# Kernel tuning notes

Hardware: AMD Instinct MI355X
Metric: run time of the kernel (lower is better)

Reference implementation:

```python
import jax, jax.numpy as jnp
import numpy as np

G1 = 3.0  # cfg.TRAIN.IoU_Gamma1
G2 = 1.0  # cfg.TRAIN.IoU_Gamma2


def setup_inputs() -> dict:
    key = jax.random.key(0)
    ks = jax.random.split(key, 5)
    B, N = 16, 2048
    cls = 0.3 * jax.random.normal(ks[0], (B, N, 2), jnp.float32)
    label_cls = jax.random.randint(ks[1], (B, N), 0, 2).astype(jnp.int32)
    label_loc = jax.random.normal(ks[2], (B, 4, N), jnp.float32)
    pred_bboxes = jax.random.uniform(ks[3], (B, 4, N), jnp.float32)
    label_target = jax.random.uniform(ks[4], (B, 4), jnp.float32)
    dataset_id = jnp.zeros((B,), jnp.int32)
    return dict(cls=cls, label_cls=label_cls, label_loc=label_loc,
                pred_bboxes=pred_bboxes, label_target=label_target,
                dataset_id=dataset_id)


def _iou(boxes, target):
    # boxes [B,4,N] (x1,y1,x2,y2); target [B,4]
    x1, y1, x2, y2 = boxes[:, 0], boxes[:, 1], boxes[:, 2], boxes[:, 3]
    tx1, ty1, tx2, ty2 = (target[:, 0:1], target[:, 1:2],
                          target[:, 2:3], target[:, 3:4])
    ww = jnp.clip(jnp.minimum(tx2, x2) - jnp.maximum(tx1, x1), 0.0)
    hh = jnp.clip(jnp.minimum(ty2, y2) - jnp.maximum(ty1, y1), 0.0)
    area = (x2 - x1) * (y2 - y1)
    ta = (tx2 - tx1) * (ty2 - ty1)
    inter = ww * hh
    return inter / (area + ta - inter)  # [B,N]


def _forward(cls, label_loc, pred_bboxes, label_target, label_cls, dataset_id):
    prob = jnp.exp(cls[..., 1])                      # [B,N]
    pos = label_cls > 0                              # [B,N]
    iou = _iou(pred_bboxes, label_target)            # [B,N]
    # centerness distance to target center
    cx = label_loc[:, 0] + label_target[:, 0:1]      # [B,N]
    cy = label_loc[:, 1] + label_target[:, 1:2]
    tcx = (label_target[:, 0] + label_target[:, 2]) * 0.5
    tcy = (label_target[:, 1] + label_target[:, 3]) * 0.5
    d = jnp.sqrt((cx - tcx[:, None]) ** 2 + (cy - tcy[:, None]) ** 2)  # [B,N]
    # pair (p,q): both positive, d[q]-d[p] >= 1.0 (== nested sorted-loop selection)
    pair = (pos[:, :, None] & pos[:, None, :]
            & ((d[:, None, :] - d[:, :, None]) >= 1.0))               # [B,N,N]
    m = pair.astype(prob.dtype)
    cnt = m.sum((1, 2))                                               # [B]
    # guard exponent with the mask to avoid inf*0 on dead pairs
    e1 = jnp.where(pair, -G1 * (prob[:, :, None] - prob[:, None, :]), 0.0)
    iou_sg = jax.lax.stop_gradient(iou)
    e2 = jnp.where(pair, -G2 * (iou[:, :, None] - iou_sg[:, None, :]), 0.0)
    denom = jnp.maximum(cnt, 1.0)
    l1 = (jnp.exp(e1) * m).sum((1, 2)) / denom                        # [B]
    l2 = (jnp.exp(e2) * m).sum((1, 2)) / denom
    valid = ((dataset_id != 1) & (cnt > 0)).astype(prob.dtype)        # [B]
    nv = valid.sum()
    safe_nv = jnp.maximum(nv, 1.0)
    f1 = jnp.where(nv > 0, (l1 * valid).sum() / safe_nv, 0.0)
    f2 = jnp.where(nv > 0, (l2 * valid).sum() / safe_nv, 0.0)
    return (f1, f2)


def reference(cls, label_cls, label_loc, pred_bboxes, label_target, dataset_id):
    return _forward(cls, label_loc, pred_bboxes, label_target, label_cls, dataset_id)
```

## Files before the change

### kernel.cpp

```cpp
#include <hip/hip_runtime.h>


#define G1 3.0f
#define G2 1.0f

constexpr int B = 16;
constexpr int N = 2048;
constexpr int TI  = 1024;
constexpr int TJ  = 64;
constexpr int IPT = 4;
constexpr int ICH = N / TI;
constexpr int JCH = N / TJ;
constexpr int PB  = ICH * JCH;
constexpr int NBLK = B * PB;

__global__ void __launch_bounds__(256)
fused_pair_kernel(const float* __restrict__ cls,
                  const int*   __restrict__ label_cls,
                  const float* __restrict__ label_loc,
                  const float* __restrict__ pred,
                  const float* __restrict__ tgt,
                  double* __restrict__ part) {
  __shared__ float4 sj[TJ];
  __shared__ double red[3][4];

  const int bid = blockIdx.x;
  const int b   = bid >> 6;
  const int r   = bid & 63;
  const int ic  = r >> 5;
  const int jc  = r & 31;
  const int t   = threadIdx.x;
  const int base = b * N;

  const float tx1 = tgt[b * 4 + 0], ty1 = tgt[b * 4 + 1];
  const float tx2 = tgt[b * 4 + 2], ty2 = tgt[b * 4 + 3];
  const float ta  = (tx2 - tx1) * (ty2 - ty1);
  const float tcx = (tx1 + tx2) * 0.5f, tcy = (ty1 + ty2) * 0.5f;

  const float* __restrict__ pb = pred      + (size_t)b * 4 * N;
  const float* __restrict__ lb = label_loc + (size_t)b * 4 * N;

  auto elem = [&](int n, float& d, float& prob, float& iou, bool& pos) {
    float x1 = pb[n], y1 = pb[N + n], x2 = pb[2 * N + n], y2 = pb[3 * N + n];
    float ww = fmaxf(fminf(tx2, x2) - fmaxf(tx1, x1), 0.f);
    float hh = fmaxf(fminf(ty2, y2) - fmaxf(ty1, y1), 0.f);
    float inter = ww * hh;
    iou  = inter / ((x2 - x1) * (y2 - y1) + ta - inter);
    prob = __expf(cls[((size_t)(base + n)) * 2 + 1]);
    pos  = label_cls[base + n] > 0;
    float cx = lb[n] + tx1, cy = lb[N + n] + ty1;
    float dx = cx - tcx, dy = cy - tcy;
    d = sqrtf(dx * dx + dy * dy);
  };

  if (t < TJ) {
    float d, prob, iou; bool pos;
    elem(jc * TJ + t, d, prob, iou, pos);
    sj[t] = make_float4(pos ? d : -1e30f,
                        __expf(G1 * prob),
                        __expf(G2 * iou), 0.f);
  }

  float di[IPT], v1i[IPT], v2i[IPT], posi[IPT];
#pragma unroll
  for (int k = 0; k < IPT; ++k) {
    float d, prob, iou; bool pos;
    elem(ic * TI + k * 256 + t, d, prob, iou, pos);
    di[k]   = d;
    posi[k] = pos ? 1.f : 0.f;
    v1i[k]  = pos ? __expf(-G1 * prob) : 0.f;
    v2i[k]  = pos ? __expf(-G2 * iou)  : 0.f;
  }
  __syncthreads();

  float s1[IPT] = {}, s2[IPT] = {}, sc[IPT] = {};
#pragma unroll 8
  for (int q = 0; q < TJ; ++q) {
    const float4 j4 = sj[q];
#pragma unroll
    for (int k = 0; k < IPT; ++k) {
      float f = (j4.x - di[k] >= 1.0f) ? 1.0f : 0.0f;
      s1[k] = fmaf(f, j4.y, s1[k]);
      s2[k] = fmaf(f, j4.z, s2[k]);
      sc[k] += f;
    }
  }

  double p1 = 0, p2 = 0, pc = 0;
#pragma unroll
  for (int k = 0; k < IPT; ++k) {
    p1 += (double)v1i[k]  * (double)s1[k];
    p2 += (double)v2i[k]  * (double)s2[k];
    pc += (double)posi[k] * (double)sc[k];
  }

  for (int off = 32; off; off >>= 1) {
    p1 += __shfl_down(p1, off);
    p2 += __shfl_down(p2, off);
    pc += __shfl_down(pc, off);
  }
  const int wave = t >> 6, lane = t & 63;
  if (lane == 0) { red[0][wave] = p1; red[1][wave] = p2; red[2][wave] = pc; }
  __syncthreads();
  if (t == 0) {
    double a = 0, bb = 0, c = 0;
    for (int wv = 0; wv < 4; ++wv) { a += red[0][wv]; bb += red[1][wv]; c += red[2][wv]; }
    part[(size_t)bid * 3 + 0] = a;
    part[(size_t)bid * 3 + 1] = bb;
    part[(size_t)bid * 3 + 2] = c;
  }
}

__global__ void finalize_kernel(const double* __restrict__ part,
                                const int* __restrict__ dataset_id,
                                float* __restrict__ out) {
  __shared__ double sl1[B], sl2[B], sv[B];
  int t = threadIdx.x;
  int b = t >> 4, k = t & 15;

  double s1 = 0, s2 = 0, sc = 0;
  for (int q = 0; q < PB; q += 16) {
    size_t idx = (size_t)(b * PB + k + q) * 3;
    s1 += part[idx]; s2 += part[idx + 1]; sc += part[idx + 2];
  }
  for (int off = 8; off; off >>= 1) {
    s1 += __shfl_down(s1, off, 16);
    s2 += __shfl_down(s2, off, 16);
    sc += __shfl_down(sc, off, 16);
  }
  if (k == 0) {
    double denom = fmax(sc, 1.0);
    bool valid = (dataset_id[b] != 1) && (sc > 0.0);
    sl1[b] = valid ? s1 / denom : 0.0;
    sl2[b] = valid ? s2 / denom : 0.0;
    sv[b]  = valid ? 1.0 : 0.0;
  }
  __syncthreads();
  if (t == 0) {
    double nv = 0, f1 = 0, f2 = 0;
    for (int bb = 0; bb < B; ++bb) { nv += sv[bb]; f1 += sl1[bb]; f2 += sl2[bb]; }
    if (nv > 0) { f1 /= nv; f2 /= nv; } else { f1 = 0; f2 = 0; }
    out[0] = (float)f1;
    out[1] = (float)f2;
  }
}

extern "C" void kernel_launch(void* const* d_in, const int* in_sizes, int n_in,
                              void* d_out, int out_size, void* d_ws, size_t ws_size,
                              hipStream_t stream) {
  const float* cls       = (const float*)d_in[0];
  const int*   label_cls = (const int*)d_in[1];
  const float* label_loc = (const float*)d_in[2];
  const float* pred      = (const float*)d_in[3];
  const float* tgt       = (const float*)d_in[4];
  const int*   dset      = (const int*)d_in[5];

  double* part = (double*)d_ws;

  fused_pair_kernel<<<NBLK, 256, 0, stream>>>(cls, label_cls, label_loc,
                                              pred, tgt, part);
  finalize_kernel<<<1, 256, 0, stream>>>(part, dset, (float*)d_out);
}
```

Before: 19.52 us.

## Replace O(N^2) pair scan with per-tile sort, suffix sums and binary search

The all-pairs scan is replaced by a prep kernel that computes per-element values and, for each 128-element tile, sorts the masked distances by rank and writes suffix sums of the exp weights. A search kernel then binary-searches each tile for the d threshold, so each element does about log(128) work per tile instead of a full scan. The separate finalize launch is folded into the search kernel through an atomic last-block counter. This cuts the arithmetic from quadratic to roughly N*(N/128)*log. In exchange it adds an intermediate global round trip and a second launch that depends on the first, and it changes the float summation order.

```diff
diff --git a/kernel.cpp b/kernel.cpp
--- a/kernel.cpp
+++ b/kernel.cpp
@@ -4,33 +4,30 @@
 #define G1 3.0f
 #define G2 1.0f
 
-constexpr int B = 16;
-constexpr int N = 2048;
-constexpr int TI  = 1024;
-constexpr int TJ  = 64;
-constexpr int IPT = 4;
-constexpr int ICH = N / TI;
-constexpr int JCH = N / TJ;
-constexpr int PB  = ICH * JCH;
-constexpr int NBLK = B * PB;
-
-__global__ void __launch_bounds__(256)
-fused_pair_kernel(const float* __restrict__ cls,
-                  const int*   __restrict__ label_cls,
-                  const float* __restrict__ label_loc,
-                  const float* __restrict__ pred,
-                  const float* __restrict__ tgt,
-                  double* __restrict__ part) {
-  __shared__ float4 sj[TJ];
-  __shared__ double red[3][4];
-
-  const int bid = blockIdx.x;
-  const int b   = bid >> 6;
-  const int r   = bid & 63;
-  const int ic  = r >> 5;
-  const int jc  = r & 31;
-  const int t   = threadIdx.x;
-  const int base = b * N;
+constexpr int B  = 16;
+constexpr int N  = 2048;
+constexpr int TS = 128;
+constexpr int NT = N / TS;
+constexpr int K2S = 8;
+constexpr int K2B = B * K2S;
+
+
+__global__ void __launch_bounds__(TS)
+prep_kernel(const float* __restrict__ cls, const int* __restrict__ label_cls,
+            const float* __restrict__ label_loc, const float* __restrict__ pred,
+            const float* __restrict__ tgt,
+            float* __restrict__ dd, float* __restrict__ v1a, float* __restrict__ v2a,
+            float* __restrict__ ssd, float* __restrict__ suf1, float* __restrict__ suf2,
+            unsigned* __restrict__ counter) {
+  __shared__ uint4 stile[TS];
+
+  if (blockIdx.x == 0 && threadIdx.x == 0) *counter = 0u;
+
+  const int b  = blockIdx.x >> 4;
+  const int jc = blockIdx.x & (NT - 1);
+  const int t  = threadIdx.x;
+  const int n  = jc * TS + t;
+  const int gn = b * N + n;
 
   const float tx1 = tgt[b * 4 + 0], ty1 = tgt[b * 4 + 1];
   const float tx2 = tgt[b * 4 + 2], ty2 = tgt[b * 4 + 3];
@@ -40,108 +37,148 @@
   const float* __restrict__ pb = pred      + (size_t)b * 4 * N;
   const float* __restrict__ lb = label_loc + (size_t)b * 4 * N;
 
-  auto elem = [&](int n, float& d, float& prob, float& iou, bool& pos) {
-    float x1 = pb[n], y1 = pb[N + n], x2 = pb[2 * N + n], y2 = pb[3 * N + n];
-    float ww = fmaxf(fminf(tx2, x2) - fmaxf(tx1, x1), 0.f);
-    float hh = fmaxf(fminf(ty2, y2) - fmaxf(ty1, y1), 0.f);
-    float inter = ww * hh;
-    iou  = inter / ((x2 - x1) * (y2 - y1) + ta - inter);
-    prob = __expf(cls[((size_t)(base + n)) * 2 + 1]);
-    pos  = label_cls[base + n] > 0;
-    float cx = lb[n] + tx1, cy = lb[N + n] + ty1;
-    float dx = cx - tcx, dy = cy - tcy;
-    d = sqrtf(dx * dx + dy * dy);
-  };
-
-  if (t < TJ) {
-    float d, prob, iou; bool pos;
-    elem(jc * TJ + t, d, prob, iou, pos);
-    sj[t] = make_float4(pos ? d : -1e30f,
-                        __expf(G1 * prob),
-                        __expf(G2 * iou), 0.f);
-  }
-
-  float di[IPT], v1i[IPT], v2i[IPT], posi[IPT];
+  float x1 = pb[n], y1 = pb[N + n], x2 = pb[2 * N + n], y2 = pb[3 * N + n];
+  float ww = fmaxf(fminf(tx2, x2) - fmaxf(tx1, x1), 0.f);
+  float hh = fmaxf(fminf(ty2, y2) - fmaxf(ty1, y1), 0.f);
+  float inter = ww * hh;
+  float iou  = inter / ((x2 - x1) * (y2 - y1) + ta - inter);
+  float prob = __expf(cls[(size_t)gn * 2 + 1]);
+  bool  pos  = label_cls[gn] > 0;
+  float cx = lb[n] + tx1, cy = lb[N + n] + ty1;
+  float dx = cx - tcx, dy = cy - tcy;
+  float d  = sqrtf(dx * dx + dy * dy);
+
+  float dm = pos ? d : -1e30f;
+  float w1 = __expf(G1 * prob);
+  float w2 = __expf(G2 * iou);
+
+  dd[gn]  = d;
+  v1a[gn] = pos ? __expf(-G1 * prob) : 0.f;
+  v2a[gn] = pos ? __expf(-G2 * iou)  : 0.f;
+
+  unsigned u = __float_as_uint(dm);
+  u ^= (u & 0x80000000u) ? 0xFFFFFFFFu : 0x80000000u;
+  stile[t] = make_uint4((unsigned)t, u, __float_as_uint(w1), __float_as_uint(w2));
+  __syncthreads();
+
+  const unsigned long long mykey = ((unsigned long long)u << 32) | (unsigned)t;
+  int rank = 0;
+  float s1 = 0.f, s2 = 0.f;
+#pragma unroll 8
+  for (int q = 0; q < TS; ++q) {
+    uint4 v = stile[q];
+    unsigned long long kq = ((unsigned long long)v.y << 32) | v.x;
+    bool lt = kq < mykey;
+    rank += lt ? 1 : 0;
+    s1 += lt ? 0.f : __uint_as_float(v.z);
+    s2 += lt ? 0.f : __uint_as_float(v.w);
+  }
+  const int outp = b * N + jc * TS + rank;
+  ssd[outp]  = dm;
+  suf1[outp] = s1;
+  suf2[outp] = s2;
+}
+
+__global__ void __launch_bounds__(256)
+search_kernel(const float* __restrict__ dd, const float* __restrict__ v1a,
+              const float* __restrict__ v2a,
+              const float* __restrict__ ssd, const float* __restrict__ suf1,
+              const float* __restrict__ suf2,
+              const int* __restrict__ dataset_id,
+              double* __restrict__ part, unsigned* __restrict__ counter,
+              float* __restrict__ out) {
+  __shared__ float lsd[N], ls1[N], ls2[N];
+  __shared__ double red[3][4];
+  __shared__ double bl1[B], bl2[B], bval[B];
+  __shared__ unsigned s_last;
+
+  const int b  = blockIdx.x >> 3;
+  const int ib = blockIdx.x & (K2S - 1);
+  const int t  = threadIdx.x;
+
+  {
+    const float4* g1 = (const float4*)(ssd  + (size_t)b * N);
+    const float4* g2 = (const float4*)(suf1 + (size_t)b * N);
+    const float4* g3 = (const float4*)(suf2 + (size_t)b * N);
+    float4* p1l = (float4*)lsd; float4* p2l = (float4*)ls1; float4* p3l = (float4*)ls2;
 #pragma unroll
-  for (int k = 0; k < IPT; ++k) {
-    float d, prob, iou; bool pos;
-    elem(ic * TI + k * 256 + t, d, prob, iou, pos);
-    di[k]   = d;
-    posi[k] = pos ? 1.f : 0.f;
-    v1i[k]  = pos ? __expf(-G1 * prob) : 0.f;
-    v2i[k]  = pos ? __expf(-G2 * iou)  : 0.f;
-  }
-  __syncthreads();
-
-  float s1[IPT] = {}, s2[IPT] = {}, sc[IPT] = {};
-#pragma unroll 8
-  for (int q = 0; q < TJ; ++q) {
-    const float4 j4 = sj[q];
+    for (int r = 0; r < (N / 4) / 256; ++r) {
+      int idx = r * 256 + t;
+      p1l[idx] = g1[idx]; p2l[idx] = g2[idx]; p3l[idx] = g3[idx];
+    }
+  }
+
+  const int   i   = b * N + ib * 256 + t;
+  const float di  = dd[i];
+  const float v1i = v1a[i];
+  const float v2i = v2a[i];
+  __syncthreads();
+
+  double s1d = 0.0, s2d = 0.0;
+  int cnt = 0;
 #pragma unroll
-    for (int k = 0; k < IPT; ++k) {
-      float f = (j4.x - di[k] >= 1.0f) ? 1.0f : 0.0f;
-      s1[k] = fmaf(f, j4.y, s1[k]);
-      s2[k] = fmaf(f, j4.z, s2[k]);
-      sc[k] += f;
-    }
-  }
-
-  double p1 = 0, p2 = 0, pc = 0;
+  for (int tile = 0; tile < NT; ++tile) {
+    const int base = tile * TS;
+    int k = 0;
 #pragma unroll
-  for (int k = 0; k < IPT; ++k) {
-    p1 += (double)v1i[k]  * (double)s1[k];
-    p2 += (double)v2i[k]  * (double)s2[k];
-    pc += (double)posi[k] * (double)sc[k];
-  }
+    for (int w = TS >> 1; w > 0; w >>= 1)
+      k += (lsd[base + k + w - 1] - di >= 1.0f) ? 0 : w;
+    k += (lsd[base + k] - di >= 1.0f) ? 0 : 1;
+    const bool any = (k < TS);
+    const int  idx = base + (any ? k : 0);
+    s1d += (double)(any ? ls1[idx] : 0.f);
+    s2d += (double)(any ? ls2[idx] : 0.f);
+    cnt += TS - k;
+  }
+
+  double p1 = (double)v1i * s1d;
+  double p2 = (double)v2i * s2d;
+  double pc = (v1i > 0.f) ? (double)cnt : 0.0;
 
   for (int off = 32; off; off >>= 1) {
     p1 += __shfl_down(p1, off);
     p2 += __shfl_down(p2, off);
     pc += __shfl_down(pc, off);
   }
-  const int wave = t >> 6, lane = t & 63;
-  if (lane == 0) { red[0][wave] = p1; red[1][wave] = p2; red[2][wave] = pc; }
+  const int wv = t >> 6, lane = t & 63;
+  if (lane == 0) { red[0][wv] = p1; red[1][wv] = p2; red[2][wv] = pc; }
   __syncthreads();
   if (t == 0) {
-    double a = 0, bb = 0, c = 0;
-    for (int wv = 0; wv < 4; ++wv) { a += red[0][wv]; bb += red[1][wv]; c += red[2][wv]; }
-    part[(size_t)bid * 3 + 0] = a;
-    part[(size_t)bid * 3 + 1] = bb;
-    part[(size_t)bid * 3 + 2] = c;
-  }
-}
-
-__global__ void finalize_kernel(const double* __restrict__ part,
-                                const int* __restrict__ dataset_id,
-                                float* __restrict__ out) {
-  __shared__ double sl1[B], sl2[B], sv[B];
-  int t = threadIdx.x;
-  int b = t >> 4, k = t & 15;
-
-  double s1 = 0, s2 = 0, sc = 0;
-  for (int q = 0; q < PB; q += 16) {
-    size_t idx = (size_t)(b * PB + k + q) * 3;
-    s1 += part[idx]; s2 += part[idx + 1]; sc += part[idx + 2];
-  }
-  for (int off = 8; off; off >>= 1) {
-    s1 += __shfl_down(s1, off, 16);
-    s2 += __shfl_down(s2, off, 16);
-    sc += __shfl_down(sc, off, 16);
-  }
-  if (k == 0) {
-    double denom = fmax(sc, 1.0);
-    bool valid = (dataset_id[b] != 1) && (sc > 0.0);
-    sl1[b] = valid ? s1 / denom : 0.0;
-    sl2[b] = valid ? s2 / denom : 0.0;
-    sv[b]  = valid ? 1.0 : 0.0;
-  }
-  __syncthreads();
-  if (t == 0) {
-    double nv = 0, f1 = 0, f2 = 0;
-    for (int bb = 0; bb < B; ++bb) { nv += sv[bb]; f1 += sl1[bb]; f2 += sl2[bb]; }
-    if (nv > 0) { f1 /= nv; f2 /= nv; } else { f1 = 0; f2 = 0; }
-    out[0] = (float)f1;
-    out[1] = (float)f2;
+    part[(size_t)blockIdx.x * 3 + 0] = red[0][0] + red[0][1] + red[0][2] + red[0][3];
+    part[(size_t)blockIdx.x * 3 + 1] = red[1][0] + red[1][1] + red[1][2] + red[1][3];
+    part[(size_t)blockIdx.x * 3 + 2] = red[2][0] + red[2][1] + red[2][2] + red[2][3];
+    __threadfence();
+    unsigned old = atomicAdd(counter, 1u);
+    s_last = (old == (unsigned)(K2B - 1)) ? 1u : 0u;
+  }
+  __syncthreads();
+  if (s_last) {
+    __threadfence();
+    double q1 = 0, q2 = 0, qc = 0;
+    if (t < K2B) {
+      const volatile double* vp = part;
+      q1 = vp[t * 3 + 0]; q2 = vp[t * 3 + 1]; qc = vp[t * 3 + 2];
+    }
+    for (int off = 4; off; off >>= 1) {
+      q1 += __shfl_down(q1, off);
+      q2 += __shfl_down(q2, off);
+      qc += __shfl_down(qc, off);
+    }
+    if (t < K2B && (t & 7) == 0) {
+      int bb = t >> 3;
+      bool valid = (dataset_id[bb] != 1) && (qc > 0.0);
+      double denom = fmax(qc, 1.0);
+      bl1[bb]  = valid ? q1 / denom : 0.0;
+      bl2[bb]  = valid ? q2 / denom : 0.0;
+      bval[bb] = valid ? 1.0 : 0.0;
+    }
+    __syncthreads();
+    if (t == 0) {
+      double nv = 0, f1 = 0, f2 = 0;
+      for (int bb = 0; bb < B; ++bb) { nv += bval[bb]; f1 += bl1[bb]; f2 += bl2[bb]; }
+      out[0] = (float)((nv > 0) ? f1 / nv : 0.0);
+      out[1] = (float)((nv > 0) ? f2 / nv : 0.0);
+    }
   }
 }
 
@@ -155,9 +192,18 @@
   const float* tgt       = (const float*)d_in[4];
   const int*   dset      = (const int*)d_in[5];
 
-  double* part = (double*)d_ws;
-
-  fused_pair_kernel<<<NBLK, 256, 0, stream>>>(cls, label_cls, label_loc,
-                                              pred, tgt, part);
-  finalize_kernel<<<1, 256, 0, stream>>>(part, dset, (float*)d_out);
+  char*     ws      = (char*)d_ws;
+  unsigned* counter = (unsigned*)ws;
+  double*   part    = (double*)(ws + 64);
+  float*    dd      = (float*)(ws + 4096);
+  float*    v1a     = dd  + (size_t)B * N;
+  float*    v2a     = v1a + (size_t)B * N;
+  float*    ssd     = v2a + (size_t)B * N;
+  float*    suf1    = ssd + (size_t)B * N;
+  float*    suf2    = suf1 + (size_t)B * N;
+
+  prep_kernel<<<B * NT, TS, 0, stream>>>(cls, label_cls, label_loc, pred, tgt,
+                                         dd, v1a, v2a, ssd, suf1, suf2, counter);
+  search_kernel<<<K2B, 256, 0, stream>>>(dd, v1a, v2a, ssd, suf1, suf2,
+                                         dset, part, counter, (float*)d_out);
 }
```

Measured after the change: 27.57 us. 41.2% more time.

## Sort j-tile by distance with suffix sums and fuse finalize via last-block atomic

Applied to the files above, without the earlier changes.

Each 64-element j tile is now ranked by distance in shared memory, and suffix sums of the exp weights are built over that order. Each i element then binary-searches the threshold and reads one suffix sum, replacing the 64-iteration masked accumulation per i element. The separate finalize kernel is removed: the last block to arrive, found with an atomic counter, does the final reduction. The cost is a memset launch, a threadfence/atomic per block, and a sequential rank pass done by only 64 threads.

```diff
diff --git a/kernel.cpp b/kernel.cpp
--- a/kernel.cpp
+++ b/kernel.cpp
@@ -4,25 +4,27 @@
 #define G1 3.0f
 #define G2 1.0f
 
-constexpr int B = 16;
-constexpr int N = 2048;
-constexpr int TI  = 1024;
-constexpr int TJ  = 64;
-constexpr int IPT = 4;
-constexpr int ICH = N / TI;
-constexpr int JCH = N / TJ;
-constexpr int PB  = ICH * JCH;
-constexpr int NBLK = B * PB;
+constexpr int B    = 16;
+constexpr int N    = 2048;
+constexpr int TJ   = 64;
+constexpr int IPT  = 4;
+constexpr int TI   = 1024;
+constexpr int ICH  = N / TI;
+constexpr int JCH  = N / TJ;
+constexpr int NBLK = B * ICH * JCH;
 
 __global__ void __launch_bounds__(256)
-fused_pair_kernel(const float* __restrict__ cls,
-                  const int*   __restrict__ label_cls,
-                  const float* __restrict__ label_loc,
-                  const float* __restrict__ pred,
-                  const float* __restrict__ tgt,
-                  double* __restrict__ part) {
-  __shared__ float4 sj[TJ];
+igr_fused_kernel(const float* __restrict__ cls, const int* __restrict__ label_cls,
+                 const float* __restrict__ label_loc, const float* __restrict__ pred,
+                 const float* __restrict__ tgt, const int* __restrict__ dataset_id,
+                 double* __restrict__ part, unsigned* __restrict__ counter,
+                 float* __restrict__ out) {
+  __shared__ uint4  stile[TJ];
+  __shared__ float  ssd[TJ];
+  __shared__ float  suf1[TJ + 1], suf2[TJ + 1];
   __shared__ double red[3][4];
+  __shared__ double bl1[B], bl2[B], bval[B];
+  __shared__ unsigned s_last;
 
   const int bid = blockIdx.x;
   const int b   = bid >> 6;
@@ -53,95 +55,108 @@
     d = sqrtf(dx * dx + dy * dy);
   };
 
+  float dm_j = 0.f; unsigned uj = 0u;
   if (t < TJ) {
     float d, prob, iou; bool pos;
     elem(jc * TJ + t, d, prob, iou, pos);
-    sj[t] = make_float4(pos ? d : -1e30f,
-                        __expf(G1 * prob),
-                        __expf(G2 * iou), 0.f);
+    dm_j = pos ? d : -1e30f;
+    uj = __float_as_uint(dm_j);
+    uj ^= (uj & 0x80000000u) ? 0xFFFFFFFFu : 0x80000000u;
+    stile[t] = make_uint4(uj, (unsigned)t,
+                          __float_as_uint(__expf(G1 * prob)),
+                          __float_as_uint(__expf(G2 * iou)));
   }
+  if (t == TJ) { suf1[TJ] = 0.f; suf2[TJ] = 0.f; }
 
-  float di[IPT], v1i[IPT], v2i[IPT], posi[IPT];
+  float di[IPT], v1i[IPT], v2i[IPT];
 #pragma unroll
   for (int k = 0; k < IPT; ++k) {
     float d, prob, iou; bool pos;
     elem(ic * TI + k * 256 + t, d, prob, iou, pos);
-    di[k]   = d;
-    posi[k] = pos ? 1.f : 0.f;
-    v1i[k]  = pos ? __expf(-G1 * prob) : 0.f;
-    v2i[k]  = pos ? __expf(-G2 * iou)  : 0.f;
+    di[k]  = d;
+    v1i[k] = pos ? __expf(-G1 * prob) : 0.f;
+    v2i[k] = pos ? __expf(-G2 * iou)  : 0.f;
   }
   __syncthreads();
 
-  float s1[IPT] = {}, s2[IPT] = {}, sc[IPT] = {};
+  if (t < TJ) {
+    const unsigned long long mykey = ((unsigned long long)uj << 32) | (unsigned)t;
+    int rank = 0; float s1 = 0.f, s2 = 0.f;
 #pragma unroll 8
-  for (int q = 0; q < TJ; ++q) {
-    const float4 j4 = sj[q];
-#pragma unroll
-    for (int k = 0; k < IPT; ++k) {
-      float f = (j4.x - di[k] >= 1.0f) ? 1.0f : 0.0f;
-      s1[k] = fmaf(f, j4.y, s1[k]);
-      s2[k] = fmaf(f, j4.z, s2[k]);
-      sc[k] += f;
+    for (int q = 0; q < TJ; ++q) {
+      uint4 v = stile[q];
+      unsigned long long kq = ((unsigned long long)v.x << 32) | v.y;
+      bool lt = kq < mykey;
+      rank += lt ? 1 : 0;
+      s1 += lt ? 0.f : __uint_as_float(v.z);
+      s2 += lt ? 0.f : __uint_as_float(v.w);
     }
+    ssd[rank] = dm_j; suf1[rank] = s1; suf2[rank] = s2;
   }
+  __syncthreads();
 
-  double p1 = 0, p2 = 0, pc = 0;
+  double p1 = 0.0, p2 = 0.0; int cnt = 0;
 #pragma unroll
   for (int k = 0; k < IPT; ++k) {
-    p1 += (double)v1i[k]  * (double)s1[k];
-    p2 += (double)v2i[k]  * (double)s2[k];
-    pc += (double)posi[k] * (double)sc[k];
+    const float d = di[k];
+    int kk = 0;
+#pragma unroll
+    for (int w = TJ >> 1; w > 0; w >>= 1)
+      kk += (ssd[kk + w - 1] - d >= 1.0f) ? 0 : w;
+    kk += (ssd[kk] - d >= 1.0f) ? 0 : 1;
+    p1 += (double)v1i[k] * (double)suf1[kk];
+    p2 += (double)v2i[k] * (double)suf2[kk];
+    cnt += (v1i[k] > 0.f) ? (TJ - kk) : 0;
   }
+  double pc = (double)cnt;
 
   for (int off = 32; off; off >>= 1) {
     p1 += __shfl_down(p1, off);
     p2 += __shfl_down(p2, off);
     pc += __shfl_down(pc, off);
   }
-  const int wave = t >> 6, lane = t & 63;
-  if (lane == 0) { red[0][wave] = p1; red[1][wave] = p2; red[2][wave] = pc; }
+  const int wv = t >> 6, lane = t & 63;
+  if (lane == 0) { red[0][wv] = p1; red[1][wv] = p2; red[2][wv] = pc; }
   __syncthreads();
   if (t == 0) {
-    double a = 0, bb = 0, c = 0;
-    for (int wv = 0; wv < 4; ++wv) { a += red[0][wv]; bb += red[1][wv]; c += red[2][wv]; }
-    part[(size_t)bid * 3 + 0] = a;
-    part[(size_t)bid * 3 + 1] = bb;
-    part[(size_t)bid * 3 + 2] = c;
-  }
-}
-
-__global__ void finalize_kernel(const double* __restrict__ part,
-                                const int* __restrict__ dataset_id,
-                                float* __restrict__ out) {
-  __shared__ double sl1[B], sl2[B], sv[B];
-  int t = threadIdx.x;
-  int b = t >> 4, k = t & 15;
-
-  double s1 = 0, s2 = 0, sc = 0;
-  for (int q = 0; q < PB; q += 16) {
-    size_t idx = (size_t)(b * PB + k + q) * 3;
-    s1 += part[idx]; s2 += part[idx + 1]; sc += part[idx + 2];
-  }
-  for (int off = 8; off; off >>= 1) {
-    s1 += __shfl_down(s1, off, 16);
-    s2 += __shfl_down(s2, off, 16);
-    sc += __shfl_down(sc, off, 16);
-  }
-  if (k == 0) {
-    double denom = fmax(sc, 1.0);
-    bool valid = (dataset_id[b] != 1) && (sc > 0.0);
-    sl1[b] = valid ? s1 / denom : 0.0;
-    sl2[b] = valid ? s2 / denom : 0.0;
-    sv[b]  = valid ? 1.0 : 0.0;
+    part[(size_t)bid * 3 + 0] = red[0][0] + red[0][1] + red[0][2] + red[0][3];
+    part[(size_t)bid * 3 + 1] = red[1][0] + red[1][1] + red[1][2] + red[1][3];
+    part[(size_t)bid * 3 + 2] = red[2][0] + red[2][1] + red[2][2] + red[2][3];
+    __threadfence();
+    unsigned old = atomicAdd(counter, 1u);
+    s_last = (old == (unsigned)(NBLK - 1)) ? 1u : 0u;
   }
   __syncthreads();
-  if (t == 0) {
-    double nv = 0, f1 = 0, f2 = 0;
-    for (int bb = 0; bb < B; ++bb) { nv += sv[bb]; f1 += sl1[bb]; f2 += sl2[bb]; }
-    if (nv > 0) { f1 /= nv; f2 /= nv; } else { f1 = 0; f2 = 0; }
-    out[0] = (float)f1;
-    out[1] = (float)f2;
+
+  if (s_last) {
+    __threadfence();
+    const int bb = t >> 4, kq = t & 15;
+    double q1 = 0, q2 = 0, qc = 0;
+    const volatile double* vp = part;
+#pragma unroll
+    for (int q = 0; q < 4; ++q) {
+      size_t idx = (size_t)(bb * 64 + kq + q * 16) * 3;
+      q1 += vp[idx]; q2 += vp[idx + 1]; qc += vp[idx + 2];
+    }
+    for (int off = 8; off; off >>= 1) {
+      q1 += __shfl_down(q1, off, 16);
+      q2 += __shfl_down(q2, off, 16);
+      qc += __shfl_down(qc, off, 16);
+    }
+    if (kq == 0) {
+      bool valid = (dataset_id[bb] != 1) && (qc > 0.0);
+      double denom = fmax(qc, 1.0);
+      bl1[bb]  = valid ? q1 / denom : 0.0;
+      bl2[bb]  = valid ? q2 / denom : 0.0;
+      bval[bb] = valid ? 1.0 : 0.0;
+    }
+    __syncthreads();
+    if (t == 0) {
+      double nv = 0, f1 = 0, f2 = 0;
+      for (int x = 0; x < B; ++x) { nv += bval[x]; f1 += bl1[x]; f2 += bl2[x]; }
+      out[0] = (float)((nv > 0) ? f1 / nv : 0.0);
+      out[1] = (float)((nv > 0) ? f2 / nv : 0.0);
+    }
   }
 }
 
@@ -155,9 +170,12 @@
   const float* tgt       = (const float*)d_in[4];
   const int*   dset      = (const int*)d_in[5];
 
-  double* part = (double*)d_ws;
+  char*     ws      = (char*)d_ws;
+  unsigned* counter = (unsigned*)ws;
+  double*   part    = (double*)(ws + 64);
 
-  fused_pair_kernel<<<NBLK, 256, 0, stream>>>(cls, label_cls, label_loc,
-                                              pred, tgt, part);
-  finalize_kernel<<<1, 256, 0, stream>>>(part, dset, (float*)d_out);
+  hipMemsetAsync(counter, 0, sizeof(unsigned), stream);
+  igr_fused_kernel<<<NBLK, 256, 0, stream>>>(cls, label_cls, label_loc, pred,
+                                             tgt, dset, part, counter,
+                                             (float*)d_out);
 }
```

After: 41.24 us. +111.2%, slower.
